# Optimization experiments

Hardware: AMD Instinct MI355X
Metric: run time of the kernel (lower is better)

## Reference

```python
import jax, jax.numpy as jnp
import numpy as np

B, L, E = 4, 1024, 1024
H, TOPK = 16, 32
DH = E // H


def setup_inputs() -> dict:
    key = jax.random.key(0)
    ks = jax.random.split(key, 11)
    s = 1.0 / np.sqrt(E)
    return {
        "Q": jax.random.normal(ks[0], (B, L, E), jnp.float32),
        "K": jax.random.normal(ks[1], (B, L, E), jnp.float32),
        "V": jax.random.normal(ks[2], (B, L, E), jnp.float32),
        "Wq": jax.random.normal(ks[3], (E, E), jnp.float32) * s,
        "bq": jnp.zeros((E,), jnp.float32),
        "Wk": jax.random.normal(ks[4], (E, E), jnp.float32) * s,
        "bk": jnp.zeros((E,), jnp.float32),
        "Wv": jax.random.normal(ks[5], (E, E), jnp.float32) * s,
        "bv": jnp.zeros((E,), jnp.float32),
        "Wo": jax.random.normal(ks[6], (E, E), jnp.float32) * s,
        "bo": jnp.zeros((E,), jnp.float32),
    }


def reference(Q, K, V, Wq, bq, Wk, bk, Wv, bv, Wo, bo):
    # Linear projections (torch Linear: x @ W.T + b), split heads -> [B,H,L,Dh]
    q = (Q @ Wq.T + bq).reshape(B, L, H, DH).transpose(0, 2, 1, 3)
    k = (K @ Wk.T + bk).reshape(B, L, H, DH).transpose(0, 2, 1, 3)
    v = (V @ Wv.T + bv).reshape(B, L, H, DH).transpose(0, 2, 1, 3)

    # Full attention logits [B,H,L,L]
    logits = jnp.einsum("bhld,bhmd->bhlm", q, k) / np.sqrt(DH)

    # Keep only top-k per query row; rest -> -inf (as in torch scatter_)
    top_vals, top_idx = jax.lax.top_k(logits, TOPK)  # [B,H,L,TOPK]
    bi = jnp.arange(B)[:, None, None, None]
    hi = jnp.arange(H)[None, :, None, None]
    li = jnp.arange(L)[None, None, :, None]
    masked = jnp.full_like(logits, -jnp.inf).at[bi, hi, li, top_idx].set(top_vals)

    attn = jax.nn.softmax(masked, axis=-1)
    out = jnp.einsum("bhlm,bhmd->bhld", attn, v)
    out = out.transpose(0, 2, 1, 3).reshape(B, L, E)
    return out @ Wo.T + bo
```

## Files before the change

### kernel.cpp

```cpp
#include <hip/hip_runtime.h>


typedef short v8s __attribute__((ext_vector_type(8)));
typedef _Float16 v8h __attribute__((ext_vector_type(8)));
typedef float v4f __attribute__((ext_vector_type(4)));

#define B_ 4
#define L_ 1024
#define E_ 1024
#define H_ 16
#define DH_ 64
#define M_ 4096

__device__ __forceinline__ unsigned short f2bf_u(float f) {
    unsigned u = __float_as_uint(f);
    unsigned r = u + 0x7FFFu + ((u >> 16) & 1u);
    return (unsigned short)(r >> 16);
}
__device__ __forceinline__ unsigned short f2h_u(float f) {
    _Float16 h = (_Float16)f;
    union { _Float16 h; unsigned short u; } c; c.h = h; return c.u;
}
__device__ __forceinline__ float h2f_u(unsigned short u) {
    union { _Float16 h; unsigned short u; } c; c.u = u; return (float)c.h;
}
__device__ __forceinline__ unsigned f2key(float f) {
    unsigned u = __float_as_uint(f);
    u = ((int)u < 0) ? ~u : (u | 0x80000000u);
    return u & 0xFFFFFFF0u;
}
__device__ __forceinline__ unsigned f2keyfull(float f) {
    unsigned u = __float_as_uint(f);
    return ((int)u < 0) ? ~u : (u | 0x80000000u);
}
__device__ __forceinline__ float key2f(unsigned k) {
    unsigned u = (k & 0x80000000u) ? (k & 0x7FFFFFFFu) : ~k;
    return __uint_as_float(u);
}
__device__ __forceinline__ float rl_f(float v, int l) {
    return __uint_as_float((unsigned)__builtin_amdgcn_readlane(__float_as_int(v), l));
}
__device__ __forceinline__ int rl_i(int v, int l) {
    return __builtin_amdgcn_readlane(v, l);
}
__device__ __forceinline__ void gload_lds16(const unsigned short* g, unsigned short* l) {
    __builtin_amdgcn_global_load_lds(
        (const __attribute__((address_space(1))) void*)g,
        (__attribute__((address_space(3))) void*)l, 16, 0, 0);
}

__global__ __launch_bounds__(256) void splitH_kernel(
    const float* __restrict__ x, unsigned short* __restrict__ y,
    int n8, int isB, float prescale)
{
    int i = blockIdx.x * 256 + threadIdx.x;
    if (i >= n8) return;
    float4 v0 = *(const float4*)(x + 8*(size_t)i);
    float4 v1 = *(const float4*)(x + 8*(size_t)i + 4);
    float f[8] = {v0.x, v0.y, v0.z, v0.w, v1.x, v1.y, v1.z, v1.w};
    unsigned short o[24];
#pragma unroll
    for (int c = 0; c < 8; ++c) {
        float fv = f[c] * prescale;
        unsigned short h = f2h_u(fv);
        float r = fv - h2f_u(h);
        unsigned short l = f2h_u(r);
        int b = 3*c;
        if (!isB) { o[b] = h; o[b+1] = l; o[b+2] = h; }
        else      { o[b] = h; o[b+1] = h; o[b+2] = l; }
    }
    uint4* dst = (uint4*)(y + 24*(size_t)i);
    const unsigned* ou = (const unsigned*)o;
    dst[0] = make_uint4(ou[0], ou[1], ou[2], ou[3]);
    dst[1] = make_uint4(ou[4], ou[5], ou[6], ou[7]);
    dst[2] = make_uint4(ou[8], ou[9], ou[10], ou[11]);
}

__global__ __launch_bounds__(512) void gemm_f16(
    const unsigned short* __restrict__ A,
    const unsigned short* __restrict__ Bw,
    const float* __restrict__ bias,
    int K2, int mode, float scale,
    float* __restrict__ outF,
    unsigned short* __restrict__ outB)
{
    __shared__ __align__(16) unsigned short As[3][128*64];
    __shared__ __align__(16) unsigned short Bs[3][128*64];
    const int t    = threadIdx.x;
    const int lane = t & 63;
    const int w    = t >> 6;
    const int quad = lane >> 4;
    const int l16  = lane & 15;
    const int bid  = blockIdx.x;
    const int xcd  = bid & 7;
    const int loc  = bid >> 3;
    const int m0   = (xcd * 4 + (loc & 3)) * 128;
    const int n0   = (loc >> 2) * 128;
    const int wrow = (w >> 1) * 32;
    const int wcol = (w & 1) * 64;

    v4f acc[2][4];
#pragma unroll
    for (int i = 0; i < 2; ++i)
#pragma unroll
        for (int j = 0; j < 4; ++j) acc[i][j] = (v4f){0.f,0.f,0.f,0.f};

#define STAGE_TILE(kt_, bi_)                                              \
  {                                                                       \
    const int k0_ = (kt_) << 6;                                           \
    _Pragma("unroll")                                                     \
    for (int c_ = 0; c_ < 2; ++c_) {                                      \
      int lin_ = c_*512 + t;                                              \
      int r_ = lin_ >> 3, s_ = lin_ & 7;                                  \
      gload_lds16(A  + (size_t)(m0 + r_)*K2 + k0_ + ((s_ ^ (r_&7))*8),    \
                  &As[bi_][lin_*8]);                                      \
    }                                                                     \
    _Pragma("unroll")                                                     \
    for (int c_ = 0; c_ < 2; ++c_) {                                      \
      int lin_ = c_*512 + t;                                              \
      int r_ = lin_ >> 3, s_ = lin_ & 7;                                  \
      gload_lds16(Bw + (size_t)(n0 + r_)*K2 + k0_ + ((s_ ^ (r_&7))*8),    \
                  &Bs[bi_][lin_*8]);                                      \
    }                                                                     \
  }

    STAGE_TILE(0, 0)
    STAGE_TILE(1, 1)

    const int nk = K2 >> 6;
    for (int ki = 0; ki < nk; ++ki) {
        const int cur = ki % 3;
        asm volatile("s_waitcnt lgkmcnt(0)" ::: "memory");
        __builtin_amdgcn_s_barrier();
        if (ki + 2 < nk) {
            const int nb = (ki + 2) % 3;
            STAGE_TILE(ki + 2, nb)
        }
        if (ki + 2 < nk)       asm volatile("s_waitcnt vmcnt(8)" ::: "memory");
        else if (ki + 1 < nk)  asm volatile("s_waitcnt vmcnt(4)" ::: "memory");
        else                   asm volatile("s_waitcnt vmcnt(0)" ::: "memory");
        __builtin_amdgcn_s_barrier();

#pragma unroll
        for (int ks = 0; ks < 2; ++ks) {
            v8h af[2], bf[4];
#pragma unroll
            for (int mt = 0; mt < 2; ++mt) {
                int ra = wrow + mt*16 + l16;
                int sl = (ks*4 + quad) ^ (ra & 7);
                af[mt] = *(const v8h*)&As[cur][ra*64 + sl*8];
            }
#pragma unroll
            for (int nt = 0; nt < 4; ++nt) {
                int rb = wcol + nt*16 + l16;
                int sl = (ks*4 + quad) ^ (rb & 7);
                bf[nt] = *(const v8h*)&Bs[cur][rb*64 + sl*8];
            }
#pragma unroll
            for (int mt = 0; mt < 2; ++mt)
#pragma unroll
                for (int nt = 0; nt < 4; ++nt)
                    acc[mt][nt] = __builtin_amdgcn_mfma_f32_16x16x32_f16(
                        af[mt], bf[nt], acc[mt][nt], 0, 0, 0);
        }
    }
#undef STAGE_TILE

#pragma unroll
    for (int nt = 0; nt < 4; ++nt) {
        int n = n0 + wcol + nt*16 + l16;
        float bb = bias[n];
#pragma unroll
        for (int mt = 0; mt < 2; ++mt) {
#pragma unroll
            for (int r = 0; r < 4; ++r) {
                int m = m0 + wrow + mt*16 + quad*4 + r;
                float val = (acc[mt][nt][r] * 0.03125f + bb) * scale;
                if (mode == 0) {
                    outF[(size_t)m * 1024 + n] = val;
                } else {
                    int b = m >> 10, l = m & 1023;
                    int h = n >> 6,  d = n & 63;
                    size_t oidx = (((size_t)(b*16 + h)) * 1024 + l) * 64 + d;
                    outF[oidx] = val;
                    if (mode == 2) outB[oidx] = f2bf_u(val);
                }
            }
        }
    }
}


#define SEL_STEP(s_, BUF)                                              \
  {                                                                    \
    v8s b0_ = BUF[0], b1_ = BUF[1];                                    \
    if ((s_) + 2 < 4) {                                                \
      BUF[0] = *(const v8s*)(kbase + ((s_)+2)*16384);                  \
      BUF[1] = *(const v8s*)(kbase + ((s_)+2)*16384 + 32);             \
    }                                                                  \
    v4f a0_ = (v4f){0.f,0.f,0.f,0.f};                                  \
    v4f a1_ = (v4f){0.f,0.f,0.f,0.f};                                  \
    a0_ = __builtin_amdgcn_mfma_f32_16x16x32_bf16(afrA[0], b0_, a0_, 0,0,0); \
    a0_ = __builtin_amdgcn_mfma_f32_16x16x32_bf16(afrA[1], b1_, a0_, 0,0,0); \
    a1_ = __builtin_amdgcn_mfma_f32_16x16x32_bf16(afrB[0], b0_, a1_, 0,0,0); \
    a1_ = __builtin_amdgcn_mfma_f32_16x16x32_bf16(afrB[1], b1_, a1_, 0,0,0); \
    if (quad < 2) {                                                    \
      _Pragma("unroll")                                                \
      for (int r_ = 0; r_ < 4; ++r_)                                   \
        sbig[(quad*4 + r_)*1044 + (s_)*256 + w*16 + l16] = a0_[r_];    \
      _Pragma("unroll")                                                \
      for (int r_ = 0; r_ < 4; ++r_)                                   \
        sbig[(8 + quad*4 + r_)*1044 + (s_)*256 + w*16 + l16] = a1_[r_];\
    }                                                                  \
  }

__global__ __launch_bounds__(1024, 4) void attn_sel(
    const unsigned short* __restrict__ qb,
    const unsigned short* __restrict__ kb,
    unsigned short* __restrict__ candB,
    unsigned* __restrict__ cntB)
{
    __shared__ __align__(16) unsigned short qbs[16*72];
    __shared__ __align__(16) float sbig[16*1044];

    const int t    = threadIdx.x;
    const int lane = t & 63;
    const int w    = t >> 6;
    const int quad = lane >> 4;
    const int l16  = lane & 15;

    const int blk = blockIdx.x;
    const int jj  = blk >> 3;
    const int bh  = (blk & 7) * 8 + (jj >> 6);
    const int qt  = jj & 63;
    const int l0  = qt * 16;
    const size_t kvB = (size_t)bh * 1024;

    if (t < 128) {
        int r2 = t >> 3, cc2 = t & 7;
        *(uint4*)&qbs[r2*72 + cc2*8] = *(const uint4*)&qb[(kvB + l0 + r2)*64 + cc2*8];
    }
    __syncthreads();
    v8s afrA[2], afrB[2];
#pragma unroll
    for (int ks = 0; ks < 2; ++ks) {
        afrA[ks] = *(const v8s*)&qbs[(l16 & 7)*72 + ks*32 + quad*8];
        afrB[ks] = *(const v8s*)&qbs[(8 + (l16 & 7))*72 + ks*32 + quad*8];
    }

    const unsigned short* kbase = kb + (kvB + w*16 + l16) * 64 + quad*8;
    v8s buf0[2], buf1[2];
    buf0[0] = *(const v8s*)(kbase);         buf0[1] = *(const v8s*)(kbase + 32);
    buf1[0] = *(const v8s*)(kbase + 16384); buf1[1] = *(const v8s*)(kbase + 16384 + 32);
    SEL_STEP(0, buf0) SEL_STEP(1, buf1)
    SEL_STEP(2, buf0) SEL_STEP(3, buf1)
    __syncthreads();

    unsigned skey[16];
#pragma unroll
    for (int kt = 0; kt < 16; ++kt) {
        float sv = sbig[w*1044 + kt*64 + lane];
        unsigned u = __float_as_uint(sv);
        u = ((int)u < 0) ? ~u : (u | 0x80000000u);
        skey[kt] = (u & 0xFFFFFFF0u) | (unsigned)kt;
    }

    unsigned kmax = 0;
#pragma unroll
    for (int kt = 0; kt < 16; ++kt) kmax = max(kmax, skey[kt]);
#pragma unroll
    for (int off = 32; off; off >>= 1)
        kmax = max(kmax, (unsigned)__shfl_xor((int)kmax, off));
    float fm = key2f(kmax);

    unsigned tau = 0; bool ok = false;
    if (fm > 0.f) {
        float lof = 0.28f * fm, hif = 0.88f * fm;
        for (int it = 0; it < 12; ++it) {
            float midf = 0.5f * (lof + hif);
            unsigned tk = f2key(midf);
            int c = 0;
#pragma unroll
            for (int kt = 0; kt < 16; ++kt)
                c += (int)__popcll(__ballot(skey[kt] >= tk));
            tau = tk;
            if (c <= 64 && c >= 36) { ok = true; break; }
            if (c > 64) lof = midf; else hif = midf;
        }
    }
    if (!ok) {
        unsigned lo = 0u, hi = 0xFFFFFFFFu;
        for (int it = 0; ; ++it) {
            unsigned mid = lo + ((hi - lo) >> 1);
            int c = 0;
#pragma unroll
            for (int kt = 0; kt < 16; ++kt)
                c += (int)__popcll(__ballot(skey[kt] >= mid));
            tau = mid;
            if (it >= 33 || (c <= 64 && c >= 36)) break;
            if (c > 64) lo = mid + 1; else hi = mid - 1;
        }
    }

    const size_t row = kvB + l0 + w;
    int base = 0;
#pragma unroll
    for (int kt = 0; kt < 16; ++kt) {
        bool f = skey[kt] >= tau;
        unsigned long long mk = __ballot(f);
        if (f) {
            int pos = base + (int)__popcll(mk & ((1ull << lane) - 1ull));
            if (pos < 64) candB[row*64 + pos] = (unsigned short)(kt*64 + lane);
        }
        base += (int)__popcll(mk);
    }
    if (lane == 0) cntB[row] = (unsigned)(base > 64 ? 64 : base);
}


#define LDGRP(base_, PV, LV)                                          \
  {                                                                   \
    _Pragma("unroll")                                                 \
    for (int u = 0; u < 8; ++u) {                                     \
      int idx_ = (base_) + u;                                         \
      float pt_ = rl_f(pc, idx_);                                     \
      int   ci_ = rl_i(cc, idx_);                                     \
      bool  vv_ = idx_ < nnz;                                         \
      PV[u] = vv_ ? pt_ : 0.f;                                        \
      LV[u] = vbase[(size_t)(vv_ ? ci_ : 0) * 64];                    \
    }                                                                 \
  }

__global__ __launch_bounds__(1024, 4) void attn_out(
    const float* __restrict__ qf,
    const float* __restrict__ kf,
    const float* __restrict__ vf,
    const unsigned short* __restrict__ candB,
    const unsigned* __restrict__ cntB,
    unsigned short* __restrict__ outX3)
{
    __shared__ __align__(16) float qfs[16*68];

    const int t    = threadIdx.x;
    const int lane = t & 63;
    const int w    = t >> 6;

    const int blk = blockIdx.x;
    const int jj  = blk >> 3;
    const int bh  = (blk & 7) * 8 + (jj >> 6);
    const int qt  = jj & 63;
    const int l0  = qt * 16;
    const size_t kvB = (size_t)bh * 1024;

    const int qrow = w;
    const size_t row = kvB + l0 + w;

    const int cnum = (int)cntB[row];
    const int cj_raw = (int)candB[row*64 + lane];

    if (t < 256) {
        int r2 = t >> 4, c4 = (t & 15) * 4;
        *(float4*)&qfs[r2*68 + c4] = *(const float4*)&qf[(kvB + l0 + r2)*64 + c4];
    }
    __syncthreads();

    int cj = 0x3FFFFFFF;
    float ef = -INFINITY;
    {
        const int cjs = (lane < cnum) ? cj_raw : 0;
        const float* kr = kf + (kvB + cjs) * 64;
        double s0 = 0.0, s1 = 0.0;
#pragma unroll
        for (int d4 = 0; d4 < 16; d4 += 2) {
            float4 qa = *(const float4*)&qfs[qrow*68 + d4*4];
            float4 ka = *(const float4*)&kr[d4*4];
            float4 qb2 = *(const float4*)&qfs[qrow*68 + d4*4 + 4];
            float4 kb2 = *(const float4*)&kr[d4*4 + 4];
            s0 += (double)qa.x * ka.x; s0 += (double)qa.y * ka.y;
            s0 += (double)qa.z * ka.z; s0 += (double)qa.w * ka.w;
            s1 += (double)qb2.x * kb2.x; s1 += (double)qb2.y * kb2.y;
            s1 += (double)qb2.z * kb2.z; s1 += (double)qb2.w * kb2.w;
        }
        if (lane < cnum) { cj = cj_raw; ef = (float)(s0 + s1); }
    }

    const unsigned uf = f2keyfull(ef);
    unsigned T = 0u;
#pragma unroll
    for (int b = 31; b >= 0; --b) {
        unsigned cndt = T | (1u << b);
        int c = (int)__popcll(__ballot(uf >= cndt));
        if (c >= 32) T = cndt;
    }
    float e31 = key2f(T);
    int c_ge = (int)__popcll(__ballot(uf >= T));

    float mx = ef;
    float tm = (uf < T) ? ef : -INFINITY;
#pragma unroll
    for (int off = 32; off; off >>= 1) {
        mx = fmaxf(mx, __shfl_xor(mx, off));
        tm = fmaxf(tm, __shfl_xor(tm, off));
    }
    float e32v = (c_ge >= 33) ? e31 : tm;

    float cmid = 0.5f * (e31 + e32v);
    const float btau = 1.5e-5f;
    bool certain = (ef > cmid + btau);
    bool band    = (fabsf(ef - cmid) <= btau);
    int A = (int)__popcll(__ballot(certain));
    int m = (int)__popcll(__ballot(band));
    float wgt = band ? ((float)(32 - A) / (float)m) : (certain ? 1.f : 0.f);

    float p = wgt * __expf(ef - mx);
    float Z = p;
#pragma unroll
    for (int off = 32; off; off >>= 1) Z += __shfl_xor(Z, off);

    bool sel = (wgt > 0.f);
    unsigned long long mk = __ballot(sel);
    int nnz = (int)__popcll(mk);
    unsigned long long lt = (1ull << lane) - 1ull;
    int pos = sel ? (int)__popcll(mk & lt)
                  : nnz + (int)__popcll(~mk & lt);
    float pc = __uint_as_float((unsigned)__builtin_amdgcn_ds_permute(
                   pos << 2, __float_as_int(p)));
    int   cc = __builtin_amdgcn_ds_permute(pos << 2, cj);

    const float* vbase = vf + kvB * 64 + lane;
    int ng = (nnz + 7) >> 3;
    float pA[8], lA[8], pB[8], lB[8];
    float oa = 0.f, ob = 0.f, oc = 0.f, od = 0.f;
    LDGRP(0, pA, lA)
    int g = 0;
    for (;;) {
        if (g + 1 < ng) LDGRP((g+1)*8, pB, lB)
        oa += pA[0]*lA[0]; ob += pA[1]*lA[1]; oc += pA[2]*lA[2]; od += pA[3]*lA[3];
        oa += pA[4]*lA[4]; ob += pA[5]*lA[5]; oc += pA[6]*lA[6]; od += pA[7]*lA[7];
        ++g; if (g >= ng) break;
        if (g + 1 < ng) LDGRP((g+1)*8, pA, lA)
        oa += pB[0]*lB[0]; ob += pB[1]*lB[1]; oc += pB[2]*lB[2]; od += pB[3]*lB[3];
        oa += pB[4]*lB[4]; ob += pB[5]*lB[5]; oc += pB[6]*lB[6]; od += pB[7]*lB[7];
        ++g; if (g >= ng) break;
    }
    float o = (oa + ob) + (oc + od);
    float oval = o / Z;

    unsigned short hh = f2h_u(oval);
    float rres = oval - h2f_u(hh);
    unsigned short ll = f2h_u(rres);
    int lq = l0 + qrow;
    size_t e = ((size_t)(bh >> 4) * 1024 + lq) * 1024 + (bh & 15) * 64 + lane;
    outX3[3*e]     = hh;
    outX3[3*e + 1] = ll;
    outX3[3*e + 2] = hh;
}

extern "C" void kernel_launch(void* const* d_in, const int* in_sizes, int n_in,
                              void* d_out, int out_size, void* d_ws, size_t ws_size,
                              hipStream_t stream)
{
    const float* Q  = (const float*)d_in[0];
    const float* K  = (const float*)d_in[1];
    const float* V  = (const float*)d_in[2];
    const float* Wq = (const float*)d_in[3];
    const float* bq = (const float*)d_in[4];
    const float* Wk = (const float*)d_in[5];
    const float* bk = (const float*)d_in[6];
    const float* Wv = (const float*)d_in[7];
    const float* bv = (const float*)d_in[8];
    const float* Wo = (const float*)d_in[9];
    const float* bo = (const float*)d_in[10];
    float* out = (float*)d_out;

    const size_t oX3 = 0;
    const size_t oW3 = 25165824;
    const size_t oQF = 31457280;
    const size_t oKF = 48234496;
    const size_t oVF = 65011712;
    const size_t oQB = 81788928;
    const size_t oKB = 90177536;
    const size_t oAO = 98566144;
    if (ws_size < 115343360) return;

    char* ws = (char*)d_ws;
    unsigned short* X3 = (unsigned short*)(ws + oX3);
    unsigned short* W3 = (unsigned short*)(ws + oW3);
    float* qf = (float*)(ws + oQF);
    float* kf = (float*)(ws + oKF);
    float* vf = (float*)(ws + oVF);
    unsigned short* qb = (unsigned short*)(ws + oQB);
    unsigned short* kb = (unsigned short*)(ws + oKB);
    unsigned short* candB = (unsigned short*)(ws + oAO);
    unsigned* cntB = (unsigned*)(ws + oAO + 8388608);

    const int nX8 = M_ * E_ / 8;
    const int nW8 = E_ * E_ / 8;
    dim3 blk(256);
    dim3 blkG(512);
    dim3 gG(256);
    dim3 gX(nX8 / 256), gW(nW8 / 256);

    splitH_kernel<<<gX, blk, 0, stream>>>(Q, X3, nX8, 0, 1.0f);
    splitH_kernel<<<gW, blk, 0, stream>>>(Wq, W3, nW8, 1, 32.0f);
    gemm_f16<<<gG, blkG, 0, stream>>>(X3, W3, bq, 3072, 2, 0.125f, qf, qb);
    splitH_kernel<<<gX, blk, 0, stream>>>(K, X3, nX8, 0, 1.0f);
    splitH_kernel<<<gW, blk, 0, stream>>>(Wk, W3, nW8, 1, 32.0f);
    gemm_f16<<<gG, blkG, 0, stream>>>(X3, W3, bk, 3072, 2, 1.0f, kf, kb);
    splitH_kernel<<<gX, blk, 0, stream>>>(V, X3, nX8, 0, 1.0f);
    splitH_kernel<<<gW, blk, 0, stream>>>(Wv, W3, nW8, 1, 32.0f);
    gemm_f16<<<gG, blkG, 0, stream>>>(X3, W3, bv, 3072, 1, 1.0f, vf, nullptr);
    attn_sel<<<dim3(4096), dim3(1024), 0, stream>>>(qb, kb, candB, cntB);
    attn_out<<<dim3(4096), dim3(1024), 0, stream>>>(qf, kf, vf, candB, cntB, X3);
    splitH_kernel<<<gW, blk, 0, stream>>>(Wo, W3, nW8, 1, 32.0f);
    gemm_f16<<<gG, blkG, 0, stream>>>(X3, W3, bo, 3072, 0, 1.0f, out, nullptr);
}
```

Before: 569.4 us.

## Batch Q and K projection GEMMs into one double-buffered launch

Adds a gemm_f16_qk kernel that computes the Q and K projections together, using a 2D grid where blockIdx.y selects the operand set. This fills the device with twice as many blocks as a single 256-block GEMM and removes one launch. The new kernel uses double-buffered LDS and launch bounds requesting higher occupancy in place of the triple-buffered pipeline. The workspace is re-laid out so both split inputs coexist, with later buffers aliasing regions that are dead by then; this risks losing latency hiding from the shallower prefetch.

```diff
diff --git a/kernel.cpp b/kernel.cpp
--- a/kernel.cpp
+++ b/kernel.cpp
@@ -75,6 +75,51 @@
     dst[1] = make_uint4(ou[4], ou[5], ou[6], ou[7]);
     dst[2] = make_uint4(ou[8], ou[9], ou[10], ou[11]);
 }
+
+#define STAGE_TILE_GEN(Ap_, Bp_, Abuf_, Bbuf_, kt_)                       \
+  {                                                                       \
+    const int k0_ = (kt_) << 6;                                           \
+    _Pragma("unroll")                                                     \
+    for (int c_ = 0; c_ < 2; ++c_) {                                      \
+      int lin_ = c_*512 + t;                                              \
+      int r_ = lin_ >> 3, s_ = lin_ & 7;                                  \
+      gload_lds16(Ap_ + (size_t)(m0 + r_)*K2 + k0_ + ((s_ ^ (r_&7))*8),   \
+                  &Abuf_[lin_*8]);                                        \
+    }                                                                     \
+    _Pragma("unroll")                                                     \
+    for (int c_ = 0; c_ < 2; ++c_) {                                      \
+      int lin_ = c_*512 + t;                                              \
+      int r_ = lin_ >> 3, s_ = lin_ & 7;                                  \
+      gload_lds16(Bp_ + (size_t)(n0 + r_)*K2 + k0_ + ((s_ ^ (r_&7))*8),   \
+                  &Bbuf_[lin_*8]);                                        \
+    }                                                                     \
+  }
+
+#define GEMM_COMPUTE(Abuf_, Bbuf_)                                        \
+  {                                                                       \
+    _Pragma("unroll")                                                     \
+    for (int ks = 0; ks < 2; ++ks) {                                      \
+        v8h af[2], bf[4];                                                 \
+        _Pragma("unroll")                                                 \
+        for (int mt = 0; mt < 2; ++mt) {                                  \
+            int ra = wrow + mt*16 + l16;                                  \
+            int sl = (ks*4 + quad) ^ (ra & 7);                            \
+            af[mt] = *(const v8h*)&Abuf_[ra*64 + sl*8];                   \
+        }                                                                 \
+        _Pragma("unroll")                                                 \
+        for (int nt = 0; nt < 4; ++nt) {                                  \
+            int rb = wcol + nt*16 + l16;                                  \
+            int sl = (ks*4 + quad) ^ (rb & 7);                            \
+            bf[nt] = *(const v8h*)&Bbuf_[rb*64 + sl*8];                   \
+        }                                                                 \
+        _Pragma("unroll")                                                 \
+        for (int mt = 0; mt < 2; ++mt)                                    \
+            _Pragma("unroll")                                             \
+            for (int nt = 0; nt < 4; ++nt)                                \
+                acc[mt][nt] = __builtin_amdgcn_mfma_f32_16x16x32_f16(     \
+                    af[mt], bf[nt], acc[mt][nt], 0, 0, 0);                \
+    }                                                                     \
+  }
 
 __global__ __launch_bounds__(512) void gemm_f16(
     const unsigned short* __restrict__ A,
@@ -105,27 +150,8 @@
 #pragma unroll
         for (int j = 0; j < 4; ++j) acc[i][j] = (v4f){0.f,0.f,0.f,0.f};
 
-#define STAGE_TILE(kt_, bi_)                                              \
-  {                                                                       \
-    const int k0_ = (kt_) << 6;                                           \
-    _Pragma("unroll")                                                     \
-    for (int c_ = 0; c_ < 2; ++c_) {                                      \
-      int lin_ = c_*512 + t;                                              \
-      int r_ = lin_ >> 3, s_ = lin_ & 7;                                  \
-      gload_lds16(A  + (size_t)(m0 + r_)*K2 + k0_ + ((s_ ^ (r_&7))*8),    \
-                  &As[bi_][lin_*8]);                                      \
-    }                                                                     \
-    _Pragma("unroll")                                                     \
-    for (int c_ = 0; c_ < 2; ++c_) {                                      \
-      int lin_ = c_*512 + t;                                              \
-      int r_ = lin_ >> 3, s_ = lin_ & 7;                                  \
-      gload_lds16(Bw + (size_t)(n0 + r_)*K2 + k0_ + ((s_ ^ (r_&7))*8),    \
-                  &Bs[bi_][lin_*8]);                                      \
-    }                                                                     \
-  }
-
-    STAGE_TILE(0, 0)
-    STAGE_TILE(1, 1)
+    STAGE_TILE_GEN(A, Bw, As[0], Bs[0], 0)
+    STAGE_TILE_GEN(A, Bw, As[1], Bs[1], 1)
 
     const int nk = K2 >> 6;
     for (int ki = 0; ki < nk; ++ki) {
@@ -134,37 +160,14 @@
         __builtin_amdgcn_s_barrier();
         if (ki + 2 < nk) {
             const int nb = (ki + 2) % 3;
-            STAGE_TILE(ki + 2, nb)
+            STAGE_TILE_GEN(A, Bw, As[nb], Bs[nb], ki + 2)
         }
         if (ki + 2 < nk)       asm volatile("s_waitcnt vmcnt(8)" ::: "memory");
         else if (ki + 1 < nk)  asm volatile("s_waitcnt vmcnt(4)" ::: "memory");
         else                   asm volatile("s_waitcnt vmcnt(0)" ::: "memory");
         __builtin_amdgcn_s_barrier();
-
-#pragma unroll
-        for (int ks = 0; ks < 2; ++ks) {
-            v8h af[2], bf[4];
-#pragma unroll
-            for (int mt = 0; mt < 2; ++mt) {
-                int ra = wrow + mt*16 + l16;
-                int sl = (ks*4 + quad) ^ (ra & 7);
-                af[mt] = *(const v8h*)&As[cur][ra*64 + sl*8];
-            }
-#pragma unroll
-            for (int nt = 0; nt < 4; ++nt) {
-                int rb = wcol + nt*16 + l16;
-                int sl = (ks*4 + quad) ^ (rb & 7);
-                bf[nt] = *(const v8h*)&Bs[cur][rb*64 + sl*8];
-            }
-#pragma unroll
-            for (int mt = 0; mt < 2; ++mt)
-#pragma unroll
-                for (int nt = 0; nt < 4; ++nt)
-                    acc[mt][nt] = __builtin_amdgcn_mfma_f32_16x16x32_f16(
-                        af[mt], bf[nt], acc[mt][nt], 0, 0, 0);
-        }
-    }
-#undef STAGE_TILE
+        GEMM_COMPUTE(As[cur], Bs[cur])
+    }
 
 #pragma unroll
     for (int nt = 0; nt < 4; ++nt) {
@@ -185,6 +188,81 @@
                     outF[oidx] = val;
                     if (mode == 2) outB[oidx] = f2bf_u(val);
                 }
+            }
+        }
+    }
+}
+
+__global__ __launch_bounds__(512, 4) void gemm_f16_qk(
+    const unsigned short* __restrict__ A0,
+    const unsigned short* __restrict__ A1,
+    const unsigned short* __restrict__ B0,
+    const unsigned short* __restrict__ B1,
+    const float* __restrict__ bias0,
+    const float* __restrict__ bias1,
+    float scale0, float scale1,
+    float* __restrict__ outF0,
+    float* __restrict__ outF1,
+    unsigned short* __restrict__ outB0,
+    unsigned short* __restrict__ outB1)
+{
+    __shared__ __align__(16) unsigned short As[2][128*64];
+    __shared__ __align__(16) unsigned short Bs[2][128*64];
+    const int K2   = 3072;
+    const int t    = threadIdx.x;
+    const int lane = t & 63;
+    const int w    = t >> 6;
+    const int quad = lane >> 4;
+    const int l16  = lane & 15;
+    const int z    = blockIdx.y;
+    const unsigned short* A  = z ? A1 : A0;
+    const unsigned short* Bw = z ? B1 : B0;
+    const float* bias        = z ? bias1 : bias0;
+    const float scale        = z ? scale1 : scale0;
+    float* outF              = z ? outF1 : outF0;
+    unsigned short* outB     = z ? outB1 : outB0;
+
+    const int bid  = blockIdx.x;
+    const int xcd  = bid & 7;
+    const int loc  = bid >> 3;
+    const int m0   = (xcd * 4 + (loc & 3)) * 128;
+    const int n0   = (loc >> 2) * 128;
+    const int wrow = (w >> 1) * 32;
+    const int wcol = (w & 1) * 64;
+
+    v4f acc[2][4];
+#pragma unroll
+    for (int i = 0; i < 2; ++i)
+#pragma unroll
+        for (int j = 0; j < 4; ++j) acc[i][j] = (v4f){0.f,0.f,0.f,0.f};
+
+    STAGE_TILE_GEN(A, Bw, As[0], Bs[0], 0)
+
+    const int nk = K2 >> 6;
+    for (int ki = 0; ki < nk; ++ki) {
+        const int cur = ki & 1;
+        __syncthreads();
+        if (ki + 1 < nk) {
+            STAGE_TILE_GEN(A, Bw, As[cur ^ 1], Bs[cur ^ 1], ki + 1)
+        }
+        GEMM_COMPUTE(As[cur], Bs[cur])
+    }
+
+#pragma unroll
+    for (int nt = 0; nt < 4; ++nt) {
+        int n = n0 + wcol + nt*16 + l16;
+        float bb = bias[n];
+#pragma unroll
+        for (int mt = 0; mt < 2; ++mt) {
+#pragma unroll
+            for (int r = 0; r < 4; ++r) {
+                int m = m0 + wrow + mt*16 + quad*4 + r;
+                float val = (acc[mt][nt][r] * 0.03125f + bb) * scale;
+                int b = m >> 10, l = m & 1023;
+                int h = n >> 6,  d = n & 63;
+                size_t oidx = (((size_t)(b*16 + h)) * 1024 + l) * 64 + d;
+                outF[oidx] = val;
+                outB[oidx] = f2bf_u(val);
             }
         }
     }
@@ -473,45 +551,40 @@
     const float* bo = (const float*)d_in[10];
     float* out = (float*)d_out;
 
-    const size_t oX3 = 0;
-    const size_t oW3 = 25165824;
-    const size_t oQF = 31457280;
-    const size_t oKF = 48234496;
-    const size_t oVF = 65011712;
-    const size_t oQB = 81788928;
-    const size_t oKB = 90177536;
-    const size_t oAO = 98566144;
     if (ws_size < 115343360) return;
 
     char* ws = (char*)d_ws;
-    unsigned short* X3 = (unsigned short*)(ws + oX3);
-    unsigned short* W3 = (unsigned short*)(ws + oW3);
-    float* qf = (float*)(ws + oQF);
-    float* kf = (float*)(ws + oKF);
-    float* vf = (float*)(ws + oVF);
-    unsigned short* qb = (unsigned short*)(ws + oQB);
-    unsigned short* kb = (unsigned short*)(ws + oKB);
-    unsigned short* candB = (unsigned short*)(ws + oAO);
-    unsigned* cntB = (unsigned*)(ws + oAO + 8388608);
+    unsigned short* X3a = (unsigned short*)(ws + 0);
+    unsigned short* X3b = (unsigned short*)(ws + 25165824);
+    float* vf = (float*)(ws + 25165824);
+    unsigned short* candB = (unsigned short*)(ws + 41943040);
+    unsigned* cntB = (unsigned*)(ws + 50331648);
+    unsigned short* W3a = (unsigned short*)(ws + 50331648);
+    unsigned short* W3b = (unsigned short*)(ws + 56623104);
+    float* qf = (float*)(ws + 62914560);
+    float* kf = (float*)(ws + 79691776);
+    unsigned short* qb = (unsigned short*)(ws + 96468992);
+    unsigned short* kb = (unsigned short*)(ws + 104857600);
 
     const int nX8 = M_ * E_ / 8;
     const int nW8 = E_ * E_ / 8;
     dim3 blk(256);
     dim3 blkG(512);
     dim3 gG(256);
+    dim3 gQK(256, 2);
     dim3 gX(nX8 / 256), gW(nW8 / 256);
 
-    splitH_kernel<<<gX, blk, 0, stream>>>(Q, X3, nX8, 0, 1.0f);
-    splitH_kernel<<<gW, blk, 0, stream>>>(Wq, W3, nW8, 1, 32.0f);
-    gemm_f16<<<gG, blkG, 0, stream>>>(X3, W3, bq, 3072, 2, 0.125f, qf, qb);
-    splitH_kernel<<<gX, blk, 0, stream>>>(K, X3, nX8, 0, 1.0f);
-    splitH_kernel<<<gW, blk, 0, stream>>>(Wk, W3, nW8, 1, 32.0f);
-    gemm_f16<<<gG, blkG, 0, stream>>>(X3, W3, bk, 3072, 2, 1.0f, kf, kb);
-    splitH_kernel<<<gX, blk, 0, stream>>>(V, X3, nX8, 0, 1.0f);
-    splitH_kernel<<<gW, blk, 0, stream>>>(Wv, W3, nW8, 1, 32.0f);
-    gemm_f16<<<gG, blkG, 0, stream>>>(X3, W3, bv, 3072, 1, 1.0f, vf, nullptr);
+    splitH_kernel<<<gX, blk, 0, stream>>>(Q, X3a, nX8, 0, 1.0f);
+    splitH_kernel<<<gX, blk, 0, stream>>>(K, X3b, nX8, 0, 1.0f);
+    splitH_kernel<<<gW, blk, 0, stream>>>(Wq, W3a, nW8, 1, 32.0f);
+    splitH_kernel<<<gW, blk, 0, stream>>>(Wk, W3b, nW8, 1, 32.0f);
+    gemm_f16_qk<<<gQK, blkG, 0, stream>>>(X3a, X3b, W3a, W3b, bq, bk,
+                                          0.125f, 1.0f, qf, kf, qb, kb);
+    splitH_kernel<<<gX, blk, 0, stream>>>(V, X3a, nX8, 0, 1.0f);
+    splitH_kernel<<<gW, blk, 0, stream>>>(Wv, W3b, nW8, 1, 32.0f);
+    gemm_f16<<<gG, blkG, 0, stream>>>(X3a, W3b, bv, 3072, 1, 1.0f, vf, nullptr);
     attn_sel<<<dim3(4096), dim3(1024), 0, stream>>>(qb, kb, candB, cntB);
-    attn_out<<<dim3(4096), dim3(1024), 0, stream>>>(qf, kf, vf, candB, cntB, X3);
-    splitH_kernel<<<gW, blk, 0, stream>>>(Wo, W3, nW8, 1, 32.0f);
-    gemm_f16<<<gG, blkG, 0, stream>>>(X3, W3, bo, 3072, 0, 1.0f, out, nullptr);
-}
+    attn_out<<<dim3(4096), dim3(1024), 0, stream>>>(qf, kf, vf, candB, cntB, X3a);
+    splitH_kernel<<<gW, blk, 0, stream>>>(Wo, W3b, nW8, 1, 32.0f);
+    gemm_f16<<<gG, blkG, 0, stream>>>(X3a, W3b, bo, 3072, 0, 1.0f, out, nullptr);
+}
```

New measurement: 513.4 us. 9.8% less time.
